# Kernel tuning notes

Measured on AMD Instinct MI355X. Metric: run time of the kernel, lower is better.

Reference implementation:

```python
import jax, jax.numpy as jnp
import numpy as np

DIM = 512
DEPTH = 6
HEADS = 8
HD = DIM // HEADS          # head dim = 64
HALF = HD // 4             # rope half_dim = 16
MLP_H = int(DIM * 4.0)
TOKENS = [1, 4, 16, 64]    # CLS, S1, S2, S3
N = sum(TOKENS)            # 85
MAX_FREQ = 10.0
BATCH = 1024
LN_EPS = 1e-5


def _build_mask():
    # CLS sees CLS+S3; each scale sees CLS+itself (block-diagonal + CLS column)
    m = np.full((N, N), -np.inf, dtype=np.float32)
    cum = np.cumsum([0] + TOKENS)  # [0,1,5,21,85]
    m[0, 0] = 0.0
    m[0, cum[3]:cum[4]] = 0.0
    for i in range(1, 4):
        s, e = cum[i], cum[i + 1]
        m[s:e, 0] = 0.0
        m[s:e, s:e] = 0.0
    return jnp.asarray(m)

MASK = _build_mask()
FREQS = jnp.exp(jnp.arange(HALF, dtype=jnp.float32) * (-np.log(MAX_FREQ) / HALF))


def _layer_norm(x, g, b):
    mu = x.mean(-1, keepdims=True)
    var = ((x - mu) ** 2).mean(-1, keepdims=True)
    return (x - mu) * jax.lax.rsqrt(var + LN_EPS) * g + b


def _rope2d(t, coords):
    # t: [B,H,P,HD], coords: [P,2] in [0,1]^2
    ang_x = coords[:, 0:1] * FREQS[None, :] * (2.0 * jnp.pi)  # [P,HALF]
    ang_y = coords[:, 1:2] * FREQS[None, :] * (2.0 * jnp.pi)
    cx, sx = jnp.cos(ang_x), jnp.sin(ang_x)
    cy, sy = jnp.cos(ang_y), jnp.sin(ang_y)
    B, H, P, _ = t.shape
    t = t.reshape(B, H, P, 4, HALF)
    x0, x1, x2, x3 = t[..., 0, :], t[..., 1, :], t[..., 2, :], t[..., 3, :]
    r = jnp.stack([x0 * cx - x1 * sx,
                   x0 * sx + x1 * cx,
                   x2 * cy - x3 * sy,
                   x2 * sy + x3 * cy], axis=3)
    return r.reshape(B, H, P, HD)


def _rope_skip_cls(t, coords):
    return jnp.concatenate([t[:, :, :1], _rope2d(t[:, :, 1:], coords)], axis=2)


def _block(x, coords, p):
    (ln1g, ln1b, qkvw, qkvb, projw, projb,
     ln2g, ln2b, f1w, f1b, f2w, f2b) = p
    B, Nn, D = x.shape
    h = _layer_norm(x, ln1g, ln1b)
    qkv = h @ qkvw + qkvb                         # [B,N,3D]
    qkv = qkv.reshape(B, Nn, 3, HEADS, HD).transpose(2, 0, 3, 1, 4)
    q, k, v = qkv[0], qkv[1], qkv[2]              # [B,H,N,HD]
    q = _rope_skip_cls(q, coords)
    k = _rope_skip_cls(k, coords)
    attn = jnp.einsum('bhqd,bhkd->bhqk', q, k) * (HD ** -0.5) + MASK
    attn = jax.nn.softmax(attn, axis=-1)
    out = jnp.einsum('bhqk,bhkd->bhqd', attn, v)
    out = out.transpose(0, 2, 1, 3).reshape(B, Nn, D)
    x = x + (out @ projw + projb)
    h = _layer_norm(x, ln2g, ln2b)
    h = jax.nn.gelu(h @ f1w + f1b, approximate=False) @ f2w + f2b
    return x + h


def setup_inputs() -> dict:
    key = jax.random.key(0)
    ks = jax.random.split(key, 8)
    s = 0.02
    nrm = lambda k, shape: jax.random.normal(k, shape, jnp.float32) * s
    return dict(
        x=jax.random.normal(ks[0], (BATCH, N, DIM), jnp.float32),
        coords=jax.random.uniform(ks[1], (N - 1, 2), jnp.float32),
        ln1_g=jnp.ones((DEPTH, DIM), jnp.float32),
        ln1_b=jnp.zeros((DEPTH, DIM), jnp.float32),
        qkv_w=nrm(ks[2], (DEPTH, DIM, 3 * DIM)),
        qkv_b=jnp.zeros((DEPTH, 3 * DIM), jnp.float32),
        proj_w=nrm(ks[3], (DEPTH, DIM, DIM)),
        proj_b=jnp.zeros((DEPTH, DIM), jnp.float32),
        ln2_g=jnp.ones((DEPTH, DIM), jnp.float32),
        ln2_b=jnp.zeros((DEPTH, DIM), jnp.float32),
        fc1_w=nrm(ks[4], (DEPTH, DIM, MLP_H)),
        fc1_b=jnp.zeros((DEPTH, MLP_H), jnp.float32),
        fc2_w=nrm(ks[5], (DEPTH, MLP_H, DIM)),
        fc2_b=jnp.zeros((DEPTH, DIM), jnp.float32),
    )


def reference(x, coords, ln1_g, ln1_b, qkv_w, qkv_b, proj_w, proj_b,
              ln2_g, ln2_b, fc1_w, fc1_b, fc2_w, fc2_b):
    for i in range(DEPTH):
        x = _block(x, coords,
                   (ln1_g[i], ln1_b[i], qkv_w[i], qkv_b[i], proj_w[i], proj_b[i],
                    ln2_g[i], ln2_b[i], fc1_w[i], fc1_b[i], fc2_w[i], fc2_b[i]))
    return x
```

## Files before the change

kernel.cpp:

```cpp
#include <hip/hip_runtime.h>
#include <hip/hip_bf16.h>
#include <math.h>

#define DIMX 512
#define NTOK 85
#define BATCH 1024
#define M_ROWS (BATCH * NTOK)
#define MLP_H 2048
#define DEPTH 6

typedef __attribute__((ext_vector_type(8))) short short8;
typedef __attribute__((ext_vector_type(4))) float f32x4;

__device__ inline float bf2f(ushort u) {
    union { unsigned int i; float f; } v; v.i = ((unsigned int)u) << 16; return v.f;
}
__device__ inline ushort f2bf(float f) {
    __hip_bfloat16 h = __float2bfloat16(f);
    union { __hip_bfloat16 h; ushort u; } v; v.h = h; return v.u;
}
__device__ inline unsigned int pack2(float a, float b) {
    return (unsigned int)f2bf(a) | ((unsigned int)f2bf(b) << 16);
}
__device__ inline float gelu_fast(float v) {
    float u = 1.5957691f * fmaf(0.044715f * v, v * v, v);
    return v / (1.0f + __expf(-u));
}

__device__ inline void gload16(const ushort* g, ushort* lds) {
    __builtin_amdgcn_global_load_lds(
        (const __attribute__((address_space(1))) unsigned int*)g,
        (__attribute__((address_space(3))) unsigned int*)lds, 16, 0, 0);
}

__global__ __launch_bounds__(256) void transpose_bf16(const float* __restrict__ in,
                                                      ushort* __restrict__ out,
                                                      int K, int N) {
    __shared__ float tile[32][33];
    int n0 = blockIdx.x * 32, k0 = blockIdx.y * 32;
    int tx = threadIdx.x, ty = threadIdx.y;
    #pragma unroll
    for (int j = 0; j < 32; j += 8)
        tile[ty + j][tx] = in[(size_t)(k0 + ty + j) * N + n0 + tx];
    __syncthreads();
    #pragma unroll
    for (int j = 0; j < 32; j += 8)
        out[(size_t)(n0 + ty + j) * K + k0 + tx] = f2bf(tile[tx][ty + j]);
}

__global__ void rope_table(const float* __restrict__ coords, float* __restrict__ tab) {
    int t = blockIdx.x;
    int idx = threadIdx.x;
    float freq = expf(-(float)idx * (2.302585093f / 16.0f));
    float twopi = 6.283185307179586f;
    float ax = coords[t * 2 + 0] * freq * twopi;
    float ay = coords[t * 2 + 1] * freq * twopi;
    tab[t * 64 + idx]      = cosf(ax);
    tab[t * 64 + 16 + idx] = sinf(ax);
    tab[t * 64 + 32 + idx] = cosf(ay);
    tab[t * 64 + 48 + idx] = sinf(ay);
}

__global__ __launch_bounds__(256) void ln_kernel(const float* __restrict__ x,
                                                 const float* __restrict__ g,
                                                 const float* __restrict__ bta,
                                                 ushort* __restrict__ out) {
    int w = threadIdx.x >> 6, lane = threadIdx.x & 63;
    size_t row = (size_t)blockIdx.x * 4 + w;
    const float* xr = x + row * DIMX;
    int c = lane * 8;
    float4 v0 = *(const float4*)(xr + c);
    float4 v1 = *(const float4*)(xr + c + 4);
    float s = v0.x + v0.y + v0.z + v0.w + v1.x + v1.y + v1.z + v1.w;
    #pragma unroll
    for (int m = 32; m; m >>= 1) s += __shfl_xor(s, m);
    float mu = s * (1.0f / 512.0f);
    float d0 = v0.x - mu, d1 = v0.y - mu, d2 = v0.z - mu, d3 = v0.w - mu;
    float d4 = v1.x - mu, d5 = v1.y - mu, d6 = v1.z - mu, d7 = v1.w - mu;
    float q = d0*d0 + d1*d1 + d2*d2 + d3*d3 + d4*d4 + d5*d5 + d6*d6 + d7*d7;
    #pragma unroll
    for (int m = 32; m; m >>= 1) q += __shfl_xor(q, m);
    float rs = rsqrtf(q * (1.0f / 512.0f) + 1e-5f);
    float4 g0 = *(const float4*)(g + c), g1 = *(const float4*)(g + c + 4);
    float4 b0 = *(const float4*)(bta + c), b1 = *(const float4*)(bta + c + 4);
    uint4 o;
    o.x = pack2(d0 * rs * g0.x + b0.x, d1 * rs * g0.y + b0.y);
    o.y = pack2(d2 * rs * g0.z + b0.z, d3 * rs * g0.w + b0.w);
    o.z = pack2(d4 * rs * g1.x + b1.x, d5 * rs * g1.y + b1.y);
    o.w = pack2(d6 * rs * g1.z + b1.z, d7 * rs * g1.w + b1.w);
    *(uint4*)&out[row * DIMX + c] = o;
}

template <int EPI>
__global__ __launch_bounds__(512, 4) void gemm_e(const ushort* __restrict__ A,
                                                 const ushort* __restrict__ Bt,
                                                 const float* __restrict__ bias,
                                                 const float* __restrict__ inF,
                                                 float* __restrict__ outF,
                                                 ushort* __restrict__ outB,
                                                 int M, int N, int K,
                                                 const float* __restrict__ tab) {
    __shared__ ushort AsF[3 * 8192] __attribute__((aligned(16)));
    __shared__ ushort BsF[3 * 4096] __attribute__((aligned(16)));
    int tid = threadIdx.x;
    int w = tid >> 6, lane = tid & 63;
    int wm = (w >> 1) * 64;
    int wn = (w & 1) * 64;

    int nbx = gridDim.x;
    int nwg = nbx * gridDim.y;
    int orig = blockIdx.y * nbx + blockIdx.x;
    int q8 = nwg >> 3, r8 = nwg & 7;
    int xcd = orig & 7, loc = orig >> 3;
    int id = (xcd < r8) ? xcd * (q8 + 1) + loc : r8 * (q8 + 1) + (xcd - r8) * q8 + loc;
    int m0 = (id / nbx) * 256;
    int n0 = (id % nbx) * 128;

    int srow = tid >> 2;
    int scol = ((tid & 3) ^ ((srow >> 1) & 3)) * 8;
    int rA0 = m0 + srow;        if (rA0 >= M) rA0 = M - 1;
    int rA1 = m0 + 128 + srow;  if (rA1 >= M) rA1 = M - 1;
    const ushort* gA0 = A + (size_t)rA0 * K + scol;
    const ushort* gA1 = A + (size_t)rA1 * K + scol;
    const ushort* gB0 = Bt + (size_t)(n0 + srow) * K + scol;
    int dwz = w * 512;
    int swA = 0, swB = 0;

#define STAGEE() do {                                                          \
        gload16(gA0, &AsF[swA + dwz]);                                         \
        gload16(gA1, &AsF[swA + 4096 + dwz]);                                  \
        gload16(gB0, &BsF[swB + dwz]);                                         \
        gA0 += 32; gA1 += 32; gB0 += 32;                                       \
        swA += 8192; if (swA == 24576) swA = 0;                                \
        swB += 4096; if (swB == 12288) swB = 0; } while (0)

    int l15 = lane & 15, lq = lane >> 4;
    int sw = (lq ^ ((l15 >> 1) & 3)) * 8;
    int aoff = (wm + l15) * 32 + sw;
    int boff = (wn + l15) * 32 + sw;
    int roffA = 0, roffB = 0;

    int NT = K >> 5;
    STAGEE(); STAGEE();

    f32x4 acc[4][4] = {};

    for (int t = 0; t < NT; ++t) {
        if (t < NT - 1) asm volatile("s_waitcnt vmcnt(3)" ::: "memory");
        else            asm volatile("s_waitcnt vmcnt(0)" ::: "memory");
        __builtin_amdgcn_s_barrier();
        short8 a[4], b[4];
        #pragma unroll
        for (int i = 0; i < 4; i++) a[i] = *(const short8*)&AsF[roffA + aoff + i * 512];
        #pragma unroll
        for (int j = 0; j < 4; j++) b[j] = *(const short8*)&BsF[roffB + boff + j * 512];
        if (t + 2 < NT) STAGEE();
        __builtin_amdgcn_s_setprio(1);
        #pragma unroll
        for (int i = 0; i < 4; i++)
            #pragma unroll
            for (int j = 0; j < 4; j++)
                acc[i][j] = __builtin_amdgcn_mfma_f32_16x16x32_bf16(a[i], b[j], acc[i][j], 0, 0, 0);
        __builtin_amdgcn_s_setprio(0);
        roffA += 8192; if (roffA == 24576) roffA = 0;
        roffB += 4096; if (roffB == 12288) roffB = 0;
    }
#undef STAGEE

    int cr = lq * 4;
    int cc = l15;
    if (EPI == 0) {
        bool ropeReg = (n0 + wn) < 1024;
        int gnb = n0 + wn + cc;
        float bb0 = bias[gnb], bb1 = bias[gnb + 16], bb2 = bias[gnb + 32], bb3 = bias[gnb + 48];
        #pragma unroll
        for (int i = 0; i < 4; i++) {
            #pragma unroll
            for (int rr = 0; rr < 4; rr++) {
                int gm = m0 + wm + i * 16 + cr + rr;
                if (gm >= M) continue;
                int n = gm % NTOK;
                float v0 = acc[i][0][rr] + bb0;
                float v1 = acc[i][1][rr] + bb1;
                float v2 = acc[i][2][rr] + bb2;
                float v3 = acc[i][3][rr] + bb3;
                if (ropeReg && n > 0) {
                    const float* tt = tab + (size_t)(n - 1) * 64 + cc;
                    float cx = tt[0], sx = tt[16], cy = tt[32], sy = tt[48];
                    float y0 = v0 * cx - v1 * sx;
                    float y1 = v0 * sx + v1 * cx;
                    float y2 = v2 * cy - v3 * sy;
                    float y3 = v2 * sy + v3 * cy;
                    v0 = y0; v1 = y1; v2 = y2; v3 = y3;
                }
                size_t o = (size_t)gm * N + gnb;
                outB[o]      = f2bf(v0);
                outB[o + 16] = f2bf(v1);
                outB[o + 32] = f2bf(v2);
                outB[o + 48] = f2bf(v3);
            }
        }
    } else {
        #pragma unroll
        for (int i = 0; i < 4; i++) {
            #pragma unroll
            for (int rr = 0; rr < 4; rr++) {
                int gm = m0 + wm + i * 16 + cr + rr;
                if (gm >= M) continue;
                #pragma unroll
                for (int j = 0; j < 4; j++) {
                    int gn = n0 + wn + j * 16 + cc;
                    float v = acc[i][j][rr] + bias[gn];
                    size_t o = (size_t)gm * N + gn;
                    if (EPI == 1) {
                        outF[o] = inF[o] + v;
                    } else {
                        outB[o] = f2bf(gelu_fast(v));
                    }
                }
            }
        }
    }
}

__global__ __launch_bounds__(384) void attn_kernel(const ushort* __restrict__ qkv,
                                                   ushort* __restrict__ out) {
    __shared__ ushort SU[13824] __attribute__((aligned(16)));
    __shared__ ushort Vt[6656]  __attribute__((aligned(16)));
    int bh = blockIdx.x;
    int b = bh >> 3, h = bh & 7;
    int tid = threadIdx.x;
    size_t base = (size_t)b * NTOK * 1536 + h * 64;

    for (int it = tid; it < 1536; it += 384) {
        int mat = (it >= 768) ? 1 : 0;
        int item = it - mat * 768;
        int n = item >> 3, g = item & 7;
        short8 v = {};
        if (n < NTOK)
            v = *(const short8*)&qkv[base + (size_t)n * 1536 + mat * 512 + g * 8];
        *(short8*)&SU[mat * 6912 + n * 72 + g * 8] = v;
    }
    for (int it = tid; it < 768; it += 384) {
        int n = it % 96;
        int d0 = (it / 96) * 8;
        short8 v = {};
        if (n < NTOK)
            v = *(const short8*)&qkv[base + (size_t)n * 1536 + 1024 + d0];
        #pragma unroll
        for (int j = 0; j < 8; j++)
            Vt[(d0 + j) * 104 + n] = (ushort)v[j];
    }
    __syncthreads();

    int wid = tid >> 6;
    int lane = tid & 63;
    int q = lane >> 4, c = lane & 15;
    int i0 = wid * 16;

    f32x4 acc[6] = {};
    #pragma unroll
    for (int kk = 0; kk < 2; kk++) {
        short8 aq = *(const short8*)&SU[(i0 + c) * 72 + kk * 32 + q * 8];
        #pragma unroll
        for (int t = 0; t < 6; t++) {
            short8 bk = *(const short8*)&SU[6912 + (t * 16 + c) * 72 + kk * 32 + q * 8];
            acc[t] = __builtin_amdgcn_mfma_f32_16x16x32_bf16(aq, bk, acc[t], 0, 0, 0);
        }
    }
    __syncthreads();

    #pragma unroll
    for (int r = 0; r < 4; r++) {
        int i = i0 + q * 4 + r;
        int si = (i == 0) ? 3 : (i < 5 ? 1 : (i < 21 ? 2 : 3));
        float vs[6];
        float m = -1e30f;
        #pragma unroll
        for (int t = 0; t < 6; t++) {
            int j = t * 16 + c;
            int sj = (j == 0) ? si : (j < 5 ? 1 : (j < 21 ? 2 : (j < NTOK ? 3 : -1)));
            float v = (sj == si) ? acc[t][r] * 0.125f : -1e30f;
            vs[t] = v;
            m = fmaxf(m, v);
        }
        #pragma unroll
        for (int mk = 8; mk; mk >>= 1) m = fmaxf(m, __shfl_xor(m, mk));
        float s = 0.f, ps[6];
        #pragma unroll
        for (int t = 0; t < 6; t++) { ps[t] = __expf(vs[t] - m); s += ps[t]; }
        #pragma unroll
        for (int mk = 8; mk; mk >>= 1) s += __shfl_xor(s, mk);
        float inv = 1.0f / s;
        #pragma unroll
        for (int t = 0; t < 6; t++)
            SU[i * 104 + t * 16 + c] = f2bf(ps[t] * inv);
    }
    __syncthreads();

    f32x4 o2[4] = {};
    #pragma unroll
    for (int kk = 0; kk < 3; kk++) {
        short8 ap = *(const short8*)&SU[(i0 + c) * 104 + kk * 32 + q * 8];
        #pragma unroll
        for (int nt = 0; nt < 4; nt++) {
            short8 bv = *(const short8*)&Vt[(nt * 16 + c) * 104 + kk * 32 + q * 8];
            o2[nt] = __builtin_amdgcn_mfma_f32_16x16x32_bf16(ap, bv, o2[nt], 0, 0, 0);
        }
    }
    size_t orow = (size_t)b * NTOK;
    #pragma unroll
    for (int nt = 0; nt < 4; nt++) {
        #pragma unroll
        for (int r = 0; r < 4; r++) {
            int i = i0 + q * 4 + r;
            if (i < NTOK)
                out[(orow + i) * DIMX + h * 64 + nt * 16 + c] = f2bf(o2[nt][r]);
        }
    }
}

extern "C" void kernel_launch(void* const* d_in, const int* in_sizes, int n_in,
                              void* d_out, int out_size, void* d_ws, size_t ws_size,
                              hipStream_t stream) {
    const float* x_in    = (const float*)d_in[0];
    const float* coords  = (const float*)d_in[1];
    const float* ln1_g   = (const float*)d_in[2];
    const float* ln1_b   = (const float*)d_in[3];
    const float* qkv_w   = (const float*)d_in[4];
    const float* qkv_b   = (const float*)d_in[5];
    const float* proj_w  = (const float*)d_in[6];
    const float* proj_b  = (const float*)d_in[7];
    const float* ln2_g   = (const float*)d_in[8];
    const float* ln2_b   = (const float*)d_in[9];
    const float* fc1_w   = (const float*)d_in[10];
    const float* fc1_b   = (const float*)d_in[11];
    const float* fc2_w   = (const float*)d_in[12];
    const float* fc2_b   = (const float*)d_in[13];

    char* ws = (char*)d_ws;
    size_t off = 0;
    auto alloc = [&](size_t bytes) -> void* {
        void* p = ws + off;
        off += (bytes + 255) & ~(size_t)255;
        return p;
    };
    auto asz = [](size_t b) { return (b + 255) & ~(size_t)255; };

    const size_t WPL = 512 * 1536 + 512 * 512 + 512 * 2048 + 2048 * 512;

    size_t fixed = asz(WPL * DEPTH * sizeof(ushort)) + asz(84 * 64 * sizeof(float));
    int Bc = 1024;
    while (Bc > 4) {
        size_t rc = (size_t)Bc * NTOK;
        size_t need = fixed + asz(rc * DIMX * sizeof(ushort)) + asz(rc * MLP_H * sizeof(ushort));
        if (need <= ws_size) break;
        Bc >>= 1;
    }
    size_t Rc = (size_t)Bc * NTOK;

    ushort* wt   = (ushort*)alloc(WPL * DEPTH * sizeof(ushort));
    float*  tab  = (float*)alloc(84 * 64 * sizeof(float));
    ushort* hbuf = (ushort*)alloc(Rc * DIMX * sizeof(ushort));
    ushort* big  = (ushort*)alloc(Rc * MLP_H * sizeof(ushort));

    rope_table<<<84, 16, 0, stream>>>(coords, tab);

    dim3 tb(32, 8);
    for (int l = 0; l < DEPTH; l++) {
        ushort* wl = wt + (size_t)l * WPL;
        transpose_bf16<<<dim3(1536 / 32, 512 / 32), tb, 0, stream>>>(
            qkv_w + (size_t)l * 512 * 1536, wl, 512, 1536);
        transpose_bf16<<<dim3(512 / 32, 512 / 32), tb, 0, stream>>>(
            proj_w + (size_t)l * 512 * 512, wl + 786432, 512, 512);
        transpose_bf16<<<dim3(2048 / 32, 512 / 32), tb, 0, stream>>>(
            fc1_w + (size_t)l * 512 * 2048, wl + 1048576, 512, 2048);
        transpose_bf16<<<dim3(512 / 32, 2048 / 32), tb, 0, stream>>>(
            fc2_w + (size_t)l * 2048 * 512, wl + 2097152, 2048, 512);
    }

    int mt256 = (int)(Rc / 256);
    int lnblocks = (int)(Rc / 4);
    for (int c = 0; c < BATCH / Bc; c++) {
        float* xc = (float*)d_out + (size_t)c * Rc * DIMX;
        const float* xin_c = x_in + (size_t)c * Rc * DIMX;
        int Mc = (int)Rc;
        for (int l = 0; l < DEPTH; l++) {
            ushort* wl = wt + (size_t)l * WPL;
            const float* xsrc = (l == 0) ? xin_c : xc;
            ln_kernel<<<lnblocks, 256, 0, stream>>>(
                xsrc, ln1_g + l * 512, ln1_b + l * 512, hbuf);
            gemm_e<0><<<dim3(1536 / 128, mt256), 512, 0, stream>>>(
                hbuf, wl, qkv_b + (size_t)l * 1536, nullptr, nullptr, big,
                Mc, 1536, 512, tab);
            attn_kernel<<<Bc * 8, 384, 0, stream>>>(big, hbuf);
            gemm_e<1><<<dim3(512 / 128, mt256), 512, 0, stream>>>(
                hbuf, wl + 786432, proj_b + (size_t)l * 512, xsrc, xc, nullptr,
                Mc, 512, 512, nullptr);
            ln_kernel<<<lnblocks, 256, 0, stream>>>(
                xc, ln2_g + l * 512, ln2_b + l * 512, hbuf);
            gemm_e<2><<<dim3(2048 / 128, mt256), 512, 0, stream>>>(
                hbuf, wl + 1048576, fc1_b + (size_t)l * 2048, nullptr, nullptr,
                big, Mc, 2048, 512, nullptr);
            gemm_e<1><<<dim3(512 / 128, mt256), 512, 0, stream>>>(
                big, wl + 2097152, fc2_b + (size_t)l * 512, xc, xc, nullptr,
                Mc, 512, 2048, nullptr);
        }
    }
}
```

Baseline: 6.671 ms.

## Add 128x128-tile GEMM with XCD-aware block remap for FC1

```diff
diff --git a/kernel.cpp b/kernel.cpp
--- a/kernel.cpp
+++ b/kernel.cpp
@@ -223,6 +223,96 @@
     }
 }
 
+template <int EPI>
+__global__ __launch_bounds__(512, 6) void gemm_f(const ushort* __restrict__ A,
+                                                 const ushort* __restrict__ Bt,
+                                                 const float* __restrict__ bias,
+                                                 const float* __restrict__ inF,
+                                                 float* __restrict__ outF,
+                                                 ushort* __restrict__ outB,
+                                                 int M, int N, int K) {
+    __shared__ ushort AsF[2 * 4096] __attribute__((aligned(16)));
+    __shared__ ushort BsF[2 * 4096] __attribute__((aligned(16)));
+    int tid = threadIdx.x;
+    int w = tid >> 6, lane = tid & 63;
+    int wm = (w >> 2) * 64;
+    int wn = (w & 3) * 32;
+
+    int nbx = gridDim.x;
+    int nwg = nbx * gridDim.y;
+    int orig = blockIdx.y * nbx + blockIdx.x;
+    int q8 = nwg >> 3, r8 = nwg & 7;
+    int xcd = orig & 7, loc = orig >> 3;
+    int id = (xcd < r8) ? xcd * (q8 + 1) + loc : r8 * (q8 + 1) + (xcd - r8) * q8 + loc;
+    int m0 = (id / nbx) * 128;
+    int n0 = (id % nbx) * 128;
+
+    int srow = tid >> 2;
+    int scol = ((tid & 3) ^ ((srow >> 1) & 3)) * 8;
+    int rA = m0 + srow; if (rA >= M) rA = M - 1;
+    const ushort* gA = A + (size_t)rA * K + scol;
+    const ushort* gB = Bt + (size_t)(n0 + srow) * K + scol;
+    int dwz = w * 512;
+    int swz = 0;
+
+#define STAGEF() do {                                                          \
+        gload16(gA, &AsF[swz + dwz]);                                          \
+        gload16(gB, &BsF[swz + dwz]);                                          \
+        gA += 32; gB += 32; swz ^= 4096; } while (0)
+
+    int l15 = lane & 15, lq = lane >> 4;
+    int sw = (lq ^ ((l15 >> 1) & 3)) * 8;
+    int aoff = (wm + l15) * 32 + sw;
+    int boff = (wn + l15) * 32 + sw;
+
+    int NT = K >> 5;
+    STAGEF();
+
+    f32x4 acc[4][2] = {};
+
+    for (int t = 0; t < NT; ++t) {
+        int roff = (t & 1) * 4096;
+        asm volatile("s_waitcnt vmcnt(0)" ::: "memory");
+        __builtin_amdgcn_s_barrier();
+        short8 a[4], b[2];
+        #pragma unroll
+        for (int i = 0; i < 4; i++) a[i] = *(const short8*)&AsF[roff + aoff + i * 512];
+        #pragma unroll
+        for (int j = 0; j < 2; j++) b[j] = *(const short8*)&BsF[roff + boff + j * 512];
+        if (t + 1 < NT) STAGEF();
+        __builtin_amdgcn_s_setprio(1);
+        #pragma unroll
+        for (int i = 0; i < 4; i++)
+            #pragma unroll
+            for (int j = 0; j < 2; j++)
+                acc[i][j] = __builtin_amdgcn_mfma_f32_16x16x32_bf16(a[i], b[j], acc[i][j], 0, 0, 0);
+        __builtin_amdgcn_s_setprio(0);
+    }
+#undef STAGEF
+
+    int cr = lq * 4;
+    int cc = l15;
+    #pragma unroll
+    for (int i = 0; i < 4; i++) {
+        #pragma unroll
+        for (int rr = 0; rr < 4; rr++) {
+            int gm = m0 + wm + i * 16 + cr + rr;
+            if (gm >= M) continue;
+            #pragma unroll
+            for (int j = 0; j < 2; j++) {
+                int gn = n0 + wn + j * 16 + cc;
+                float v = acc[i][j][rr] + bias[gn];
+                size_t o = (size_t)gm * N + gn;
+                if (EPI == 1) {
+                    outF[o] = inF[o] + v;
+                } else {
+                    outB[o] = f2bf(gelu_fast(v));
+                }
+            }
+        }
+    }
+}
+
 __global__ __launch_bounds__(384) void attn_kernel(const ushort* __restrict__ qkv,
                                                    ushort* __restrict__ out) {
     __shared__ ushort SU[13824] __attribute__((aligned(16)));
@@ -380,6 +470,7 @@
     }
 
     int mt256 = (int)(Rc / 256);
+    int mt128 = (int)(Rc / 128);
     int lnblocks = (int)(Rc / 4);
     for (int c = 0; c < BATCH / Bc; c++) {
         float* xc = (float*)d_out + (size_t)c * Rc * DIMX;
@@ -399,9 +490,9 @@
                 Mc, 512, 512, nullptr);
             ln_kernel<<<lnblocks, 256, 0, stream>>>(
                 xc, ln2_g + l * 512, ln2_b + l * 512, hbuf);
-            gemm_e<2><<<dim3(2048 / 128, mt256), 512, 0, stream>>>(
+            gemm_f<2><<<dim3(2048 / 128, mt128), 512, 0, stream>>>(
                 hbuf, wl + 1048576, fc1_b + (size_t)l * 2048, nullptr, nullptr,
-                big, Mc, 2048, 512, nullptr);
+                big, Mc, 2048, 512);
             gemm_e<1><<<dim3(512 / 128, mt256), 512, 0, stream>>>(
                 big, wl + 2097152, fc2_b + (size_t)l * 512, xc, xc, nullptr,
                 Mc, 512, 2048, nullptr);
```

Result: no change. 6.718 ms (+0.7%).

## Fold LayerNorm into GEMM epilogues via weight scaling and residual row stats

Applied to the files above, without the earlier changes.

```diff
diff --git a/kernel.cpp b/kernel.cpp
--- a/kernel.cpp
+++ b/kernel.cpp
@@ -31,21 +31,6 @@
     __builtin_amdgcn_global_load_lds(
         (const __attribute__((address_space(1))) unsigned int*)g,
         (__attribute__((address_space(3))) unsigned int*)lds, 16, 0, 0);
-}
-
-__global__ __launch_bounds__(256) void transpose_bf16(const float* __restrict__ in,
-                                                      ushort* __restrict__ out,
-                                                      int K, int N) {
-    __shared__ float tile[32][33];
-    int n0 = blockIdx.x * 32, k0 = blockIdx.y * 32;
-    int tx = threadIdx.x, ty = threadIdx.y;
-    #pragma unroll
-    for (int j = 0; j < 32; j += 8)
-        tile[ty + j][tx] = in[(size_t)(k0 + ty + j) * N + n0 + tx];
-    __syncthreads();
-    #pragma unroll
-    for (int j = 0; j < 32; j += 8)
-        out[(size_t)(n0 + ty + j) * K + k0 + tx] = f2bf(tile[tx][ty + j]);
 }
 
 __global__ void rope_table(const float* __restrict__ coords, float* __restrict__ tab) {
@@ -61,10 +46,45 @@
     tab[t * 64 + 48 + idx] = sinf(ay);
 }
 
-__global__ __launch_bounds__(256) void ln_kernel(const float* __restrict__ x,
-                                                 const float* __restrict__ g,
-                                                 const float* __restrict__ bta,
-                                                 ushort* __restrict__ out) {
+__global__ __launch_bounds__(256) void transpose_bf16(const float* __restrict__ in,
+                                                      ushort* __restrict__ out,
+                                                      int K, int N,
+                                                      const float* __restrict__ sc) {
+    __shared__ float tile[32][33];
+    int n0 = blockIdx.x * 32, k0 = blockIdx.y * 32;
+    int tx = threadIdx.x, ty = threadIdx.y;
+    #pragma unroll
+    for (int j = 0; j < 32; j += 8)
+        tile[ty + j][tx] = in[(size_t)(k0 + ty + j) * N + n0 + tx];
+    __syncthreads();
+    float s = sc ? sc[k0 + tx] : 1.0f;
+    #pragma unroll
+    for (int j = 0; j < 32; j += 8)
+        out[(size_t)(n0 + ty + j) * K + k0 + tx] = f2bf(tile[tx][ty + j] * s);
+}
+
+__global__ __launch_bounds__(256) void colaff_kernel(const float* __restrict__ W,
+                                                     const float* __restrict__ g,
+                                                     const float* __restrict__ be,
+                                                     const float* __restrict__ bias,
+                                                     float* __restrict__ c1,
+                                                     float* __restrict__ c2,
+                                                     int K, int N) {
+    int n = blockIdx.x * 256 + threadIdx.x;
+    if (n >= N) return;
+    float a = 0.f, b = 0.f;
+    for (int k = 0; k < K; k++) {
+        float w = W[(size_t)k * N + n];
+        a = fmaf(g[k], w, a);
+        b = fmaf(be[k], w, b);
+    }
+    c1[n] = a;
+    c2[n] = b + bias[n];
+}
+
+__global__ __launch_bounds__(256) void stats_conv(const float* __restrict__ x,
+                                                  ushort* __restrict__ xb,
+                                                  float* __restrict__ part) {
     int w = threadIdx.x >> 6, lane = threadIdx.x & 63;
     size_t row = (size_t)blockIdx.x * 4 + w;
     const float* xr = x + row * DIMX;
@@ -72,29 +92,32 @@
     float4 v0 = *(const float4*)(xr + c);
     float4 v1 = *(const float4*)(xr + c + 4);
     float s = v0.x + v0.y + v0.z + v0.w + v1.x + v1.y + v1.z + v1.w;
-    #pragma unroll
-    for (int m = 32; m; m >>= 1) s += __shfl_xor(s, m);
-    float mu = s * (1.0f / 512.0f);
-    float d0 = v0.x - mu, d1 = v0.y - mu, d2 = v0.z - mu, d3 = v0.w - mu;
-    float d4 = v1.x - mu, d5 = v1.y - mu, d6 = v1.z - mu, d7 = v1.w - mu;
-    float q = d0*d0 + d1*d1 + d2*d2 + d3*d3 + d4*d4 + d5*d5 + d6*d6 + d7*d7;
-    #pragma unroll
-    for (int m = 32; m; m >>= 1) q += __shfl_xor(q, m);
-    float rs = rsqrtf(q * (1.0f / 512.0f) + 1e-5f);
-    float4 g0 = *(const float4*)(g + c), g1 = *(const float4*)(g + c + 4);
-    float4 b0 = *(const float4*)(bta + c), b1 = *(const float4*)(bta + c + 4);
+    float q = v0.x*v0.x + v0.y*v0.y + v0.z*v0.z + v0.w*v0.w
+            + v1.x*v1.x + v1.y*v1.y + v1.z*v1.z + v1.w*v1.w;
+    #pragma unroll
+    for (int m = 32; m; m >>= 1) { s += __shfl_xor(s, m); q += __shfl_xor(q, m); }
     uint4 o;
-    o.x = pack2(d0 * rs * g0.x + b0.x, d1 * rs * g0.y + b0.y);
-    o.y = pack2(d2 * rs * g0.z + b0.z, d3 * rs * g0.w + b0.w);
-    o.z = pack2(d4 * rs * g1.x + b1.x, d5 * rs * g1.y + b1.y);
-    o.w = pack2(d6 * rs * g1.z + b1.z, d7 * rs * g1.w + b1.w);
-    *(uint4*)&out[row * DIMX + c] = o;
+    o.x = pack2(v0.x, v0.y); o.y = pack2(v0.z, v0.w);
+    o.z = pack2(v1.x, v1.y); o.w = pack2(v1.z, v1.w);
+    *(uint4*)&xb[row * DIMX + c] = o;
+    if (lane == 0) {
+        float4* pp = (float4*)&part[row * 16];
+        pp[0] = (float4){s, q, 0.f, 0.f};
+        pp[1] = (float4){0.f, 0.f, 0.f, 0.f};
+        pp[2] = (float4){0.f, 0.f, 0.f, 0.f};
+        pp[3] = (float4){0.f, 0.f, 0.f, 0.f};
+    }
 }
 
 template <int EPI>
 __global__ __launch_bounds__(512, 4) void gemm_e(const ushort* __restrict__ A,
                                                  const ushort* __restrict__ Bt,
                                                  const float* __restrict__ bias,
+                                                 const float* __restrict__ cc1,
+                                                 const float* __restrict__ cc2,
+                                                 const float* __restrict__ statsIn,
+                                                 float* __restrict__ statsOut,
+                                                 ushort* __restrict__ xbOut,
                                                  const float* __restrict__ inF,
                                                  float* __restrict__ outF,
                                                  ushort* __restrict__ outB,
@@ -169,53 +192,89 @@
 
     int cr = lq * 4;
     int cc = l15;
-    if (EPI == 0) {
-        bool ropeReg = (n0 + wn) < 1024;
-        int gnb = n0 + wn + cc;
-        float bb0 = bias[gnb], bb1 = bias[gnb + 16], bb2 = bias[gnb + 32], bb3 = bias[gnb + 48];
+    int gnb = n0 + wn + cc;
+    if (EPI == 0 || EPI == 2) {
+        float c1_0 = cc1[gnb], c1_1 = cc1[gnb + 16], c1_2 = cc1[gnb + 32], c1_3 = cc1[gnb + 48];
+        float c2_0 = cc2[gnb], c2_1 = cc2[gnb + 16], c2_2 = cc2[gnb + 32], c2_3 = cc2[gnb + 48];
+        bool ropeReg = (EPI == 0) && ((n0 + wn) < 1024);
         #pragma unroll
         for (int i = 0; i < 4; i++) {
             #pragma unroll
             for (int rr = 0; rr < 4; rr++) {
                 int gm = m0 + wm + i * 16 + cr + rr;
                 if (gm >= M) continue;
-                int n = gm % NTOK;
-                float v0 = acc[i][0][rr] + bb0;
-                float v1 = acc[i][1][rr] + bb1;
-                float v2 = acc[i][2][rr] + bb2;
-                float v3 = acc[i][3][rr] + bb3;
-                if (ropeReg && n > 0) {
-                    const float* tt = tab + (size_t)(n - 1) * 64 + cc;
-                    float cx = tt[0], sx = tt[16], cy = tt[32], sy = tt[48];
-                    float y0 = v0 * cx - v1 * sx;
-                    float y1 = v0 * sx + v1 * cx;
-                    float y2 = v2 * cy - v3 * sy;
-                    float y3 = v2 * sy + v3 * cy;
-                    v0 = y0; v1 = y1; v2 = y2; v3 = y3;
+                const float4* pp = (const float4*)&statsIn[(size_t)gm * 16];
+                float4 p0 = pp[0], p1 = pp[1], p2 = pp[2], p3 = pp[3];
+                float s1 = p0.x + p0.z + p1.x + p1.z + p2.x + p2.z + p3.x + p3.z;
+                float s2 = p0.y + p0.w + p1.y + p1.w + p2.y + p2.w + p3.y + p3.w;
+                float mu = s1 * (1.0f / 512.0f);
+                float var = fmaf(-mu, mu, s2 * (1.0f / 512.0f));
+                float rs = rsqrtf(var + 1e-5f);
+                float rm = -rs * mu;
+                float v0 = fmaf(rs, acc[i][0][rr], fmaf(rm, c1_0, c2_0));
+                float v1 = fmaf(rs, acc[i][1][rr], fmaf(rm, c1_1, c2_1));
+                float v2 = fmaf(rs, acc[i][2][rr], fmaf(rm, c1_2, c2_2));
+                float v3 = fmaf(rs, acc[i][3][rr], fmaf(rm, c1_3, c2_3));
+                if (EPI == 0) {
+                    int n = gm % NTOK;
+                    if (ropeReg && n > 0) {
+                        const float* tt = tab + (size_t)(n - 1) * 64 + cc;
+                        float cx = tt[0], sx = tt[16], cy = tt[32], sy = tt[48];
+                        float y0 = v0 * cx - v1 * sx;
+                        float y1 = v0 * sx + v1 * cx;
+                        float y2 = v2 * cy - v3 * sy;
+                        float y3 = v2 * sy + v3 * cy;
+                        v0 = y0; v1 = y1; v2 = y2; v3 = y3;
+                    }
+                    size_t o = (size_t)gm * N + gnb;
+                    outB[o]      = f2bf(v0);
+                    outB[o + 16] = f2bf(v1);
+                    outB[o + 32] = f2bf(v2);
+                    outB[o + 48] = f2bf(v3);
+                } else {
+                    size_t o = (size_t)gm * N + gnb;
+                    outB[o]      = f2bf(gelu_fast(v0));
+                    outB[o + 16] = f2bf(gelu_fast(v1));
+                    outB[o + 32] = f2bf(gelu_fast(v2));
+                    outB[o + 48] = f2bf(gelu_fast(v3));
                 }
-                size_t o = (size_t)gm * N + gnb;
-                outB[o]      = f2bf(v0);
-                outB[o + 16] = f2bf(v1);
-                outB[o + 32] = f2bf(v2);
-                outB[o + 48] = f2bf(v3);
             }
         }
     } else {
+        float bb0 = bias[gnb], bb1 = bias[gnb + 16], bb2 = bias[gnb + 32], bb3 = bias[gnb + 48];
+        int stripe = (n0 + wn) >> 6;
+        bool emit = (statsOut != nullptr);
         #pragma unroll
         for (int i = 0; i < 4; i++) {
             #pragma unroll
             for (int rr = 0; rr < 4; rr++) {
                 int gm = m0 + wm + i * 16 + cr + rr;
                 if (gm >= M) continue;
-                #pragma unroll
-                for (int j = 0; j < 4; j++) {
-                    int gn = n0 + wn + j * 16 + cc;
-                    float v = acc[i][j][rr] + bias[gn];
-                    size_t o = (size_t)gm * N + gn;
-                    if (EPI == 1) {
-                        outF[o] = inF[o] + v;
-                    } else {
-                        outB[o] = f2bf(gelu_fast(v));
+                size_t o = (size_t)gm * N + gnb;
+                float o0 = inF[o]      + acc[i][0][rr] + bb0;
+                float o1 = inF[o + 16] + acc[i][1][rr] + bb1;
+                float o2 = inF[o + 32] + acc[i][2][rr] + bb2;
+                float o3 = inF[o + 48] + acc[i][3][rr] + bb3;
+                outF[o]      = o0;
+                outF[o + 16] = o1;
+                outF[o + 32] = o2;
+                outF[o + 48] = o3;
+                if (emit) {
+                    xbOut[o]      = f2bf(o0);
+                    xbOut[o + 16] = f2bf(o1);
+                    xbOut[o + 32] = f2bf(o2);
+                    xbOut[o + 48] = f2bf(o3);
+                    float s1 = o0 + o1 + o2 + o3;
+                    float s2 = o0*o0 + o1*o1 + o2*o2 + o3*o3;
+                    #pragma unroll
+                    for (int mk = 1; mk < 16; mk <<= 1) {
+                        s1 += __shfl_xor(s1, mk);
+                        s2 += __shfl_xor(s2, mk);
+                    }
+                    if (l15 == 0) {
+                        float* pd = &statsOut[(size_t)gm * 16 + stripe * 2];
+                        pd[0] = s1;
+                        pd[1] = s2;
                     }
                 }
             }
@@ -348,12 +407,17 @@
     auto asz = [](size_t b) { return (b + 255) & ~(size_t)255; };
 
     const size_t WPL = 512 * 1536 + 512 * 512 + 512 * 2048 + 2048 * 512;
-
-    size_t fixed = asz(WPL * DEPTH * sizeof(ushort)) + asz(84 * 64 * sizeof(float));
+    const size_t CAFF_L = 2 * 1536 + 2 * 2048;
+
+    size_t fixed = asz(WPL * DEPTH * sizeof(ushort)) + asz(84 * 64 * sizeof(float))
+                 + asz(CAFF_L * DEPTH * sizeof(float));
     int Bc = 1024;
     while (Bc > 4) {
         size_t rc = (size_t)Bc * NTOK;
-        size_t need = fixed + asz(rc * DIMX * sizeof(ushort)) + asz(rc * MLP_H * sizeof(ushort));
+        size_t need = fixed
+                    + 3 * asz(rc * DIMX * sizeof(ushort))
+                    + asz(rc * MLP_H * sizeof(ushort))
+                    + 2 * asz(rc * 16 * sizeof(float));
         if (need <= ws_size) break;
         Bc >>= 1;
     }
@@ -361,50 +425,61 @@
 
     ushort* wt   = (ushort*)alloc(WPL * DEPTH * sizeof(ushort));
     float*  tab  = (float*)alloc(84 * 64 * sizeof(float));
+    float*  caff = (float*)alloc(CAFF_L * DEPTH * sizeof(float));
     ushort* hbuf = (ushort*)alloc(Rc * DIMX * sizeof(ushort));
+    ushort* xb1  = (ushort*)alloc(Rc * DIMX * sizeof(ushort));
+    ushort* xb2  = (ushort*)alloc(Rc * DIMX * sizeof(ushort));
     ushort* big  = (ushort*)alloc(Rc * MLP_H * sizeof(ushort));
+    float*  part1 = (float*)alloc(Rc * 16 * sizeof(float));
+    float*  part2 = (float*)alloc(Rc * 16 * sizeof(float));
 
     rope_table<<<84, 16, 0, stream>>>(coords, tab);
 
     dim3 tb(32, 8);
     for (int l = 0; l < DEPTH; l++) {
         ushort* wl = wt + (size_t)l * WPL;
+        float* cl = caff + (size_t)l * CAFF_L;
         transpose_bf16<<<dim3(1536 / 32, 512 / 32), tb, 0, stream>>>(
-            qkv_w + (size_t)l * 512 * 1536, wl, 512, 1536);
+            qkv_w + (size_t)l * 512 * 1536, wl, 512, 1536, ln1_g + l * 512);
         transpose_bf16<<<dim3(512 / 32, 512 / 32), tb, 0, stream>>>(
-            proj_w + (size_t)l * 512 * 512, wl + 786432, 512, 512);
+            proj_w + (size_t)l * 512 * 512, wl + 786432, 512, 512, nullptr);
         transpose_bf16<<<dim3(2048 / 32, 512 / 32), tb, 0, stream>>>(
-            fc1_w + (size_t)l * 512 * 2048, wl + 1048576, 512, 2048);
+            fc1_w + (size_t)l * 512 * 2048, wl + 1048576, 512, 2048, ln2_g + l * 512);
         transpose_bf16<<<dim3(512 / 32, 2048 / 32), tb, 0, stream>>>(
-            fc2_w + (size_t)l * 2048 * 512, wl + 2097152, 2048, 512);
+            fc2_w + (size_t)l * 2048 * 512, wl + 2097152, 2048, 512, nullptr);
+        colaff_kernel<<<6, 256, 0, stream>>>(
+            qkv_w + (size_t)l * 512 * 1536, ln1_g + l * 512, ln1_b + l * 512,
+            qkv_b + (size_t)l * 1536, cl, cl + 1536, 512, 1536);
+        colaff_kernel<<<8, 256, 0, stream>>>(
+            fc1_w + (size_t)l * 512 * 2048, ln2_g + l * 512, ln2_b + l * 512,
+            fc1_b + (size_t)l * 2048, cl + 3072, cl + 5120, 512, 2048);
     }
 
     int mt256 = (int)(Rc / 256);
-    int lnblocks = (int)(Rc / 4);
     for (int c = 0; c < BATCH / Bc; c++) {
         float* xc = (float*)d_out + (size_t)c * Rc * DIMX;
         const float* xin_c = x_in + (size_t)c * Rc * DIMX;
         int Mc = (int)Rc;
+        stats_conv<<<(int)(Rc / 4), 256, 0, stream>>>(xin_c, xb1, part1);
         for (int l = 0; l < DEPTH; l++) {
             ushort* wl = wt + (size_t)l * WPL;
+            float* cl = caff + (size_t)l * CAFF_L;
             const float* xsrc = (l == 0) ? xin_c : xc;
-            ln_kernel<<<lnblocks, 256, 0, stream>>>(
-                xsrc, ln1_g + l * 512, ln1_b + l * 512, hbuf);
             gemm_e<0><<<dim3(1536 / 128, mt256), 512, 0, stream>>>(
-                hbuf, wl, qkv_b + (size_t)l * 1536, nullptr, nullptr, big,
-                Mc, 1536, 512, tab);
+                xb1, wl, nullptr, cl, cl + 1536, part1, nullptr, nullptr,
+                nullptr, nullptr, big, Mc, 1536, 512, tab);
             attn_kernel<<<Bc * 8, 384, 0, stream>>>(big, hbuf);
             gemm_e<1><<<dim3(512 / 128, mt256), 512, 0, stream>>>(
-                hbuf, wl + 786432, proj_b + (size_t)l * 512, xsrc, xc, nullptr,
-                Mc, 512, 512, nullptr);
-            ln_kernel<<<lnblocks, 256, 0, stream>>>(
-                xc, ln2_g + l * 512, ln2_b + l * 512, hbuf);
+                hbuf, wl + 786432, proj_b + (size_t)l * 512, nullptr, nullptr,
+                nullptr, part2, xb2, xsrc, xc, nullptr, Mc, 512, 512, nullptr);
             gemm_e<2><<<dim3(2048 / 128, mt256), 512, 0, stream>>>(
-                hbuf, wl + 1048576, fc1_b + (size_t)l * 2048, nullptr, nullptr,
-                big, Mc, 2048, 512, nullptr);
+                xb2, wl + 1048576, nullptr, cl + 3072, cl + 5120, part2,
+                nullptr, nullptr, nullptr, nullptr, big, Mc, 2048, 512, nullptr);
+            bool last = (l == DEPTH - 1);
             gemm_e<1><<<dim3(512 / 128, mt256), 512, 0, stream>>>(
-                big, wl + 2097152, fc2_b + (size_t)l * 512, xc, xc, nullptr,
-                Mc, 512, 2048, nullptr);
-        }
-    }
-}
+                big, wl + 2097152, fc2_b + (size_t)l * 512, nullptr, nullptr,
+                nullptr, last ? nullptr : part1, last ? nullptr : xb1,
+                xc, xc, nullptr, Mc, 512, 2048, nullptr);
+        }
+    }
+}
```

New measurement: 8.823 ms. +32.3%, slower.
